# Optimization experiments

Measured on AMD Instinct MI355X. Metric: run time of the kernel, lower is better.

Reference implementation:

```python
import jax, jax.numpy as jnp
import numpy as np

NUM_HEADS = 16
HEAD_DIM = 64  # hidden_size 1024 / 16 heads


def setup_inputs() -> dict:
    key = jax.random.key(0)
    ks = jax.random.split(key, 7)
    B, S, D = 32, 577, 1024
    s = 0.02
    return {
        "hidden_states": jax.random.normal(ks[0], (B, S, D), dtype=jnp.float32),
        "Wq": jax.random.normal(ks[1], (D, D), dtype=jnp.float32) * s,
        "bq": jax.random.normal(ks[2], (D,), dtype=jnp.float32) * s,
        "Wk": jax.random.normal(ks[3], (D, D), dtype=jnp.float32) * s,
        "bk": jax.random.normal(ks[4], (D,), dtype=jnp.float32) * s,
        "Wv": jax.random.normal(ks[5], (D, D), dtype=jnp.float32) * s,
        "bv": jax.random.normal(ks[6], (D,), dtype=jnp.float32) * s,
    }


def _split_heads(x):
    # [B, S, D] -> [B, H, S, d]
    B, S, D = x.shape
    return x.reshape(B, S, NUM_HEADS, HEAD_DIM).transpose(0, 2, 1, 3)


def reference(hidden_states, Wq, bq, Wk, bk, Wv, bv):
    # torch Linear: y = x @ W^T + b
    q = _split_heads(hidden_states @ Wq.T + bq)  # [B,H,S,d]
    k = _split_heads(hidden_states @ Wk.T + bk)
    v = _split_heads(hidden_states @ Wv.T + bv)

    scale = 1.0 / np.sqrt(HEAD_DIM).astype(np.float32)
    scores = jnp.einsum("bhqd,bhkd->bhqk", q, k) * scale  # [B,H,S,S]
    probs = jax.nn.softmax(scores, axis=-1)
    ctx = jnp.einsum("bhqk,bhkd->bhqd", probs, v)  # [B,H,S,d]
    B, H, S, d = ctx.shape
    ctx = ctx.transpose(0, 2, 1, 3).reshape(B, S, H * d)  # [B,S,D]
    return ctx
```

## Files before the change

kernel.cpp:

```cpp
#include <hip/hip_runtime.h>
#include <stdint.h>

#define NB 32
#define SEQ 577
#define SPAD 640
#define NH 16
#define HD 64
#define DM 1024
#define MTOT (NB * SEQ)
#define KT_N 16

typedef __bf16 bf16x8 __attribute__((ext_vector_type(8)));
typedef float f32x4 __attribute__((ext_vector_type(4)));
typedef unsigned short u16x8 __attribute__((ext_vector_type(8)));
typedef unsigned short u16x4 __attribute__((ext_vector_type(4)));

__device__ __forceinline__ unsigned short f2bf(float f) {
  unsigned int u = __builtin_bit_cast(unsigned int, f);
  return (unsigned short)((u + 0x7FFFu + ((u >> 16) & 1u)) >> 16);
}

__device__ __forceinline__ f32x4 mfma16(bf16x8 a, bf16x8 b, f32x4 c) {
  return __builtin_amdgcn_mfma_f32_16x16x32_bf16(a, b, c, 0, 0, 0);
}

__device__ __forceinline__ void gload16(const unsigned short* g, unsigned short* l) {
  __builtin_amdgcn_global_load_lds(
      (const __attribute__((address_space(1))) unsigned int*)g,
      (__attribute__((address_space(3))) unsigned int*)l, 16, 0, 0);
}

#define BC8(p) __builtin_bit_cast(bf16x8, *(const u16x8*)(p))

#if __has_builtin(__builtin_amdgcn_exp2f)
#define EXP2(x) __builtin_amdgcn_exp2f(x)
#else
#define EXP2(x) exp2f(x)
#endif

__global__ void cvt_kernel(const float* __restrict__ x,
                           const float* __restrict__ wq,
                           const float* __restrict__ wk,
                           const float* __restrict__ wv,
                           unsigned short* __restrict__ xb,
                           unsigned short* __restrict__ wb) {
  const long long NX = (long long)MTOT * DM;
  long long i = ((long long)blockIdx.x * blockDim.x + threadIdx.x) * 4;
  const float* src;
  unsigned short* dst;
  if (i < NX) {
    src = x + i;
    dst = xb + i;
  } else {
    long long j = i - NX;
    int wsel = (int)(j >> 20);
    long long off = j & 0xFFFFF;
    src = (wsel == 0 ? wq : wsel == 1 ? wk : wv) + off;
    dst = wb + j;
  }
  f32x4 v = *(const f32x4*)src;
  u16x4 o;
  o.x = f2bf(v.x); o.y = f2bf(v.y); o.z = f2bf(v.z); o.w = f2bf(v.w);
  *(u16x4*)dst = o;
}

template <int MODE>
__device__ __forceinline__ void kloop256(
    unsigned short* LDS, const unsigned short* const* gA,
    const unsigned short* const* gB, f32x4 (&acc)[8][4],
    int rA0, int rB0, int ch0, int ch1) {
#define MM(ACC, AF, BF)                                   \
  do {                                                    \
    if constexpr (MODE == 0)                              \
      ACC = mfma16(AF, BF, ACC);                          \
    else                                                  \
      ACC = mfma16(BF, AF, ACC);                          \
  } while (0)
  const int t = threadIdx.x;
  for (int kt = 0; kt < KT_N; ++kt) {
    unsigned short* ab = LDS + (kt & 1) * 32768;
    unsigned short* bb = ab + 16384;
    const bool st = (kt + 2) < KT_N;
    const int ko2 = (kt + 2) * 64;
    bf16x8 af[4][2], bf0[2][2], bf1[2][2];

#pragma unroll
    for (int mi = 0; mi < 4; mi++) {
      const unsigned short* rp = ab + (rA0 + mi * 16) * 64;
      af[mi][0] = BC8(rp + ch0);
      af[mi][1] = BC8(rp + ch1);
    }
#pragma unroll
    for (int ni = 0; ni < 2; ni++) {
      const unsigned short* rp = bb + (rB0 + ni * 16) * 64;
      bf0[ni][0] = BC8(rp + ch0);
      bf0[ni][1] = BC8(rp + ch1);
    }
    __builtin_amdgcn_s_setprio(1);
#pragma unroll
    for (int mi = 0; mi < 4; mi++)
#pragma unroll
      for (int ni = 0; ni < 2; ni++) {
        MM(acc[mi][ni], af[mi][0], bf0[ni][0]);
        MM(acc[mi][ni], af[mi][1], bf0[ni][1]);
      }
    __builtin_amdgcn_s_setprio(0);
    asm volatile("s_waitcnt lgkmcnt(0)" ::: "memory");
    __builtin_amdgcn_s_barrier();
    __builtin_amdgcn_sched_barrier(0);

    if (st) {
      gload16(gA[0] + ko2, ab + 0 * 4096 + t * 8);
      gload16(gA[2] + ko2, ab + 2 * 4096 + t * 8);
    }
#pragma unroll
    for (int ni = 0; ni < 2; ni++) {
      const unsigned short* rp = bb + (rB0 + (2 + ni) * 16) * 64;
      bf1[ni][0] = BC8(rp + ch0);
      bf1[ni][1] = BC8(rp + ch1);
    }
    __builtin_amdgcn_s_setprio(1);
#pragma unroll
    for (int mi = 0; mi < 4; mi++)
#pragma unroll
      for (int ni = 0; ni < 2; ni++) {
        MM(acc[mi][2 + ni], af[mi][0], bf1[ni][0]);
        MM(acc[mi][2 + ni], af[mi][1], bf1[ni][1]);
      }
    __builtin_amdgcn_s_setprio(0);
    asm volatile("s_waitcnt lgkmcnt(0)" ::: "memory");
    __builtin_amdgcn_s_barrier();
    __builtin_amdgcn_sched_barrier(0);

    if (st) {
#pragma unroll
      for (int q = 0; q < 4; q++) gload16(gB[q] + ko2, bb + q * 4096 + t * 8);
    }
#pragma unroll
    for (int mi = 0; mi < 4; mi++) {
      const unsigned short* rp = ab + (rA0 + 64 + mi * 16) * 64;
      af[mi][0] = BC8(rp + ch0);
      af[mi][1] = BC8(rp + ch1);
    }
    __builtin_amdgcn_s_setprio(1);
#pragma unroll
    for (int mi = 0; mi < 4; mi++)
#pragma unroll
      for (int ni = 0; ni < 2; ni++) {
        MM(acc[4 + mi][2 + ni], af[mi][0], bf1[ni][0]);
        MM(acc[4 + mi][2 + ni], af[mi][1], bf1[ni][1]);
      }
    __builtin_amdgcn_s_setprio(0);
    asm volatile("s_waitcnt lgkmcnt(0)" ::: "memory");
    __builtin_amdgcn_s_barrier();
    __builtin_amdgcn_sched_barrier(0);

    if (st) {
      gload16(gA[1] + ko2, ab + 1 * 4096 + t * 8);
      gload16(gA[3] + ko2, ab + 3 * 4096 + t * 8);
    }
    __builtin_amdgcn_s_setprio(1);
#pragma unroll
    for (int mi = 0; mi < 4; mi++)
#pragma unroll
      for (int ni = 0; ni < 2; ni++) {
        MM(acc[4 + mi][ni], af[mi][0], bf0[ni][0]);
        MM(acc[4 + mi][ni], af[mi][1], bf0[ni][1]);
      }
    __builtin_amdgcn_s_setprio(0);
    if (kt == KT_N - 2)
      asm volatile("s_waitcnt vmcnt(0)" ::: "memory");
    else
      asm volatile("s_waitcnt vmcnt(8)" ::: "memory");
    __builtin_amdgcn_s_barrier();
    __builtin_amdgcn_sched_barrier(0);
  }
#undef MM
}

__global__ __launch_bounds__(512, 2) void gemm256u(
    const unsigned short* __restrict__ xb, const unsigned short* __restrict__ wb,
    const float* __restrict__ bq, const float* __restrict__ bk,
    const float* __restrict__ bv,
    unsigned short* __restrict__ qo, unsigned short* __restrict__ ko,
    unsigned short* __restrict__ vo) {
  __shared__ __align__(16) unsigned short LDS[65536];
  const int id = blockIdx.x;
  int m_tile, col, z;
  bool modeV;
  if (id < 584) {
    modeV = false;
    const int xcd = id & 7, j = id >> 3;
    const int p = xcd * 73 + j;
    m_tile = p >> 3;
    col = p & 7;
    z = col >> 2;
  } else {
    modeV = true;
    const int q = id - 584;
    const int xcd = q & 7, j = q >> 3;
    const int p = (xcd < 4) ? xcd * 37 + j : 148 + (xcd - 4) * 36 + j;
    m_tile = p >> 2;
    col = p & 3;
    z = 2;
  }
  const int n0 = (modeV ? col : (col & 3)) * 256;
  const int m0 = m_tile * 256;

  const int t = threadIdx.x;
  const int lane = t & 63;
  const int w = t >> 6;
  const int g = lane >> 4, c = lane & 15;
  const int wm = w & 1, wn = w >> 1;

  const unsigned short* W = wb + (size_t)z * (DM * DM);
  const float* bias = modeV ? bv : (z ? bk : bq);
  unsigned short* outp = modeV ? vo : (z ? ko : qo);

  const int srow = t >> 3;
  const int schunk = (t & 7) ^ (srow & 7);
  const unsigned short* gA[4];
#pragma unroll
  for (int q = 0; q < 4; q++) {
    int rg = m0 + q * 64 + srow;
    if (rg > MTOT - 1) rg = MTOT - 1;
    gA[q] = xb + (size_t)rg * DM + schunk * 8;
  }
  const unsigned short* gB[4];
#pragma unroll
  for (int q = 0; q < 4; q++)
    gB[q] = W + (size_t)(n0 + q * 64 + srow) * DM + schunk * 8;

  const int cx = c & 7;
  const int ch0 = (g ^ cx) * 8;
  const int ch1 = ((4 + g) ^ cx) * 8;

  f32x4 acc[8][4];
#pragma unroll
  for (int mi = 0; mi < 8; mi++)
#pragma unroll
    for (int ni = 0; ni < 4; ni++) acc[mi][ni] = (f32x4)0.0f;

#pragma unroll
  for (int q = 0; q < 4; q++) gload16(gA[q], LDS + q * 4096 + t * 8);
#pragma unroll
  for (int q = 0; q < 4; q++) gload16(gB[q], LDS + 16384 + q * 4096 + t * 8);
#pragma unroll
  for (int q = 0; q < 4; q++) gload16(gA[q] + 64, LDS + 32768 + q * 4096 + t * 8);
#pragma unroll
  for (int q = 0; q < 4; q++)
    gload16(gB[q] + 64, LDS + 32768 + 16384 + q * 4096 + t * 8);
  asm volatile("s_waitcnt vmcnt(8)" ::: "memory");
  __builtin_amdgcn_s_barrier();
  __builtin_amdgcn_sched_barrier(0);

  const int rA0 = wm * 128 + c;
  const int rB0 = wn * 64 + c;

  if (!modeV)
    kloop256<0>(LDS, gA, gB, acc, rA0, rB0, ch0, ch1);
  else
    kloop256<1>(LDS, gA, gB, acc, rA0, rB0, ch0, ch1);

  if (!modeV) {
    float bias4[4];
#pragma unroll
    for (int ni = 0; ni < 4; ni++) bias4[ni] = bias[n0 + wn * 64 + ni * 16 + c];
#pragma unroll
    for (int mi = 0; mi < 8; mi++) {
      int mb = m0 + wm * 128 + mi * 16 + g * 4;
#pragma unroll
      for (int r = 0; r < 4; r++) {
        int m = mb + r;
        if (m >= MTOT) continue;
        int bi = m / SEQ;
        int s = m - bi * SEQ;
#pragma unroll
        for (int ni = 0; ni < 4; ni++) {
          int n = n0 + wn * 64 + ni * 16 + c;
          int hh = n >> 6, dd = n & 63;
          outp[(((size_t)bi * NH + hh) * SPAD + s) * HD + dd] =
              f2bf(acc[mi][ni][r] + bias4[ni]);
        }
      }
    }
  } else {
#pragma unroll
    for (int ni = 0; ni < 4; ni++) {
#pragma unroll
      for (int r = 0; r < 4; r++) {
        int n = n0 + wn * 64 + ni * 16 + g * 4 + r;
        int hh = n >> 6, dd = n & 63;
        float bn = bias[n];
#pragma unroll
        for (int mi = 0; mi < 8; mi++) {
          int m = m0 + wm * 128 + mi * 16 + c;
          if (m >= MTOT) continue;
          int bi = m / SEQ;
          int s = m - bi * SEQ;
          outp[(((size_t)bi * NH + hh) * HD + dd) * SPAD + s] =
              f2bf(acc[mi][ni][r] + bn);
        }
      }
    }
  }
}

__global__ __launch_bounds__(256, 4) void attn_kernel(
    const unsigned short* __restrict__ Qb, const unsigned short* __restrict__ Kb,
    const unsigned short* __restrict__ Vt, float* __restrict__ out) {
  __shared__ __align__(16) unsigned short Ks[64 * 64];
  __shared__ __align__(16) unsigned short Vs[80 * 64];
  __shared__ __align__(16) unsigned short Pl[4][16 * 72];
  const int t = threadIdx.x, lane = t & 63, w = t >> 6;
  const int g = lane >> 4, c = lane & 15;

  const int id = blockIdx.x;
  const int xcd = id & 7;
  const int slot = id >> 3;
  const int qt = slot % 10;
  const int pairIdx = slot / 10;
  const int pair = xcd * 64 + pairIdx;
  const int b = pair >> 4;
  const int h = pair & 15;

  const int q0 = qt * 64 + w * 16;
  const size_t bh = (size_t)b * NH + h;
  const unsigned short* Qp = Qb + bh * SPAD * HD;
  const unsigned short* Kp = Kb + bh * SPAD * HD;
  const unsigned short* Vp = Vt + bh * HD * SPAD;

  {
    int rr = t >> 4, col = (t & 15) * 4;
    unsigned short val = (rr == 0) ? (unsigned short)0x3F80 : (unsigned short)0;
    u16x4 v4 = {val, val, val, val};
    *(u16x4*)(Vs + (64 + rr) * 64 + col) = v4;
  }

  bf16x8 qf0 = __builtin_bit_cast(
      bf16x8, *(const u16x8*)(Qp + (size_t)(q0 + c) * HD + g * 8));
  bf16x8 qf1 = __builtin_bit_cast(
      bf16x8, *(const u16x8*)(Qp + (size_t)(q0 + c) * HD + 32 + g * 8));

  const int C0 = t, C1 = t + 256;
  const int r0 = C0 >> 3, cg0 = (C0 & 7) ^ (r0 & 7);
  const int r1 = C1 >> 3, cg1 = (C1 & 7) ^ (r1 & 7);
  const unsigned short* gK0 = Kp + (size_t)(r0 * 8 + cg0) * 8;
  const unsigned short* gK1 = Kp + (size_t)(r1 * 8 + cg1) * 8;
  const unsigned short* gV0 = Vp + (size_t)r0 * SPAD + cg0 * 8;
  const unsigned short* gV1 = Vp + (size_t)r1 * SPAD + cg1 * 8;
  unsigned short* lK0 = Ks + C0 * 8;
  unsigned short* lK1 = Ks + C1 * 8;
  unsigned short* lV0 = Vs + C0 * 8;
  unsigned short* lV1 = Vs + C1 * 8;

  f32x4 oacc[5];
#pragma unroll
  for (int nt = 0; nt < 5; nt++) oacc[nt] = (f32x4)0.0f;
  unsigned short* pl = &Pl[w][0];
  const float SC = 0.125f * 1.44269504f;

  for (int kt = 0; kt < 10; kt++) {
    const int kv0 = kt * 64;
    __syncthreads();
    gload16(gK0 + kv0 * 64, lK0);
    gload16(gK1 + kv0 * 64, lK1);
    gload16(gV0 + kv0, lV0);
    gload16(gV1 + kv0, lV1);
    __syncthreads();

    f32x4 sc[4];
#pragma unroll
    for (int nt = 0; nt < 4; nt++) {
      const int row = nt * 16 + c;
      const unsigned short* kb = Ks + row * 64;
      bf16x8 k0 = __builtin_bit_cast(
          bf16x8, *(const u16x8*)(kb + ((g ^ (row & 7)) * 8)));
      bf16x8 k1 = __builtin_bit_cast(
          bf16x8, *(const u16x8*)(kb + (((4 + g) ^ (row & 7)) * 8)));
      sc[nt] = mfma16(qf0, k0, (f32x4)0.0f);
      sc[nt] = mfma16(qf1, k1, sc[nt]);
    }

    if (kt == 9) {
#pragma unroll
      for (int nt = 0; nt < 4; nt++) {
        const bool valid = (kv0 + nt * 16 + c) < SEQ;
#pragma unroll
        for (int r = 0; r < 4; r++)
          sc[nt][r] = valid ? EXP2(sc[nt][r] * SC) : 0.0f;
      }
    } else {
#pragma unroll
      for (int nt = 0; nt < 4; nt++)
#pragma unroll
        for (int r = 0; r < 4; r++) sc[nt][r] = EXP2(sc[nt][r] * SC);
    }

#pragma unroll
    for (int nt = 0; nt < 4; nt++)
#pragma unroll
      for (int r = 0; r < 4; r++)
        pl[(g * 4 + r) * 72 + nt * 16 + c] = f2bf(sc[nt][r]);
    bf16x8 pa0 = __builtin_bit_cast(bf16x8, *(const u16x8*)(pl + c * 72 + g * 8));
    bf16x8 pa1 =
        __builtin_bit_cast(bf16x8, *(const u16x8*)(pl + c * 72 + 32 + g * 8));

#pragma unroll
    for (int nt = 0; nt < 5; nt++) {
      const int row = nt * 16 + c;
      const unsigned short* vb = Vs + row * 64;
      bf16x8 v0 = __builtin_bit_cast(
          bf16x8, *(const u16x8*)(vb + ((g ^ (row & 7)) * 8)));
      bf16x8 v1 = __builtin_bit_cast(
          bf16x8, *(const u16x8*)(vb + (((4 + g) ^ (row & 7)) * 8)));
      oacc[nt] = mfma16(pa0, v0, oacc[nt]);
      oacc[nt] = mfma16(pa1, v1, oacc[nt]);
    }
  }

#pragma unroll
  for (int r = 0; r < 4; r++) {
    int s = q0 + g * 4 + r;
    if (s >= SEQ) continue;
    float l = __shfl(oacc[4][r], lane & 48, 64);
    float inv = 1.0f / l;
#pragma unroll
    for (int nt = 0; nt < 4; nt++)
      out[((size_t)b * SEQ + s) * DM + h * HD + nt * 16 + c] =
          oacc[nt][r] * inv;
  }
}

extern "C" void kernel_launch(void* const* d_in, const int* in_sizes, int n_in,
                              void* d_out, int out_size, void* d_ws,
                              size_t ws_size, hipStream_t stream) {
  const float* x = (const float*)d_in[0];
  const float* Wq = (const float*)d_in[1];
  const float* bq = (const float*)d_in[2];
  const float* Wk = (const float*)d_in[3];
  const float* bk = (const float*)d_in[4];
  const float* Wv = (const float*)d_in[5];
  const float* bv = (const float*)d_in[6];
  float* out = (float*)d_out;

  const size_t nXB = (size_t)MTOT * DM;
  const size_t nWB = (size_t)3 * DM * DM;
  const size_t nQK = (size_t)NB * NH * SPAD * HD;
  const size_t needed = (nXB + nWB + 3 * nQK) * 2;
  if (ws_size < needed) return;

  unsigned short* xb = (unsigned short*)d_ws;
  unsigned short* wb = xb + nXB;
  unsigned short* Qb = wb + nWB;
  unsigned short* Kb = Qb + nQK;
  unsigned short* Vt = Kb + nQK;

  cvt_kernel<<<21536, 256, 0, stream>>>(x, Wq, Wk, Wv, xb, wb);
  gemm256u<<<876, 512, 0, stream>>>(xb, wb, bq, bk, bv, Qb, Kb, Vt);
  attn_kernel<<<5120, 256, 0, stream>>>(Qb, Kb, Vt, out);
}
```

Measured before the change: 385.7 us.

## Double-buffer K/V tiles in attention kernel to overlap loads with MFMA

The attention kernel keeps two LDS buffers each for K and V. It prefetches the next 64-key tile while the current tile is used for QK^T, exp and PV, so the two barriers per iteration become one barrier at the end. The ones-row block used to accumulate the softmax denominator moves to its own LDS array, since it no longer sits at the end of Vs. LDS use per block grows, so the launch bounds target drops from 4 to 3 blocks per CU. That trades occupancy for hiding global-load latency.

```diff
diff --git a/kernel.cpp b/kernel.cpp
--- a/kernel.cpp
+++ b/kernel.cpp
@@ -306,11 +306,12 @@
   }
 }
 
-__global__ __launch_bounds__(256, 4) void attn_kernel(
+__global__ __launch_bounds__(256, 3) void attn_kernel(
     const unsigned short* __restrict__ Qb, const unsigned short* __restrict__ Kb,
     const unsigned short* __restrict__ Vt, float* __restrict__ out) {
-  __shared__ __align__(16) unsigned short Ks[64 * 64];
-  __shared__ __align__(16) unsigned short Vs[80 * 64];
+  __shared__ __align__(16) unsigned short Ks[2][64 * 64];
+  __shared__ __align__(16) unsigned short Vs[2][64 * 64];
+  __shared__ __align__(16) unsigned short Vones[16 * 64];
   __shared__ __align__(16) unsigned short Pl[4][16 * 72];
   const int t = threadIdx.x, lane = t & 63, w = t >> 6;
   const int g = lane >> 4, c = lane & 15;
@@ -334,7 +335,7 @@
     int rr = t >> 4, col = (t & 15) * 4;
     unsigned short val = (rr == 0) ? (unsigned short)0x3F80 : (unsigned short)0;
     u16x4 v4 = {val, val, val, val};
-    *(u16x4*)(Vs + (64 + rr) * 64 + col) = v4;
+    *(u16x4*)(Vones + rr * 64 + col) = v4;
   }
 
   bf16x8 qf0 = __builtin_bit_cast(
@@ -349,10 +350,6 @@
   const unsigned short* gK1 = Kp + (size_t)(r1 * 8 + cg1) * 8;
   const unsigned short* gV0 = Vp + (size_t)r0 * SPAD + cg0 * 8;
   const unsigned short* gV1 = Vp + (size_t)r1 * SPAD + cg1 * 8;
-  unsigned short* lK0 = Ks + C0 * 8;
-  unsigned short* lK1 = Ks + C1 * 8;
-  unsigned short* lV0 = Vs + C0 * 8;
-  unsigned short* lV1 = Vs + C1 * 8;
 
   f32x4 oacc[5];
 #pragma unroll
@@ -360,20 +357,27 @@
   unsigned short* pl = &Pl[w][0];
   const float SC = 0.125f * 1.44269504f;
 
+  gload16(gK0, Ks[0] + C0 * 8);
+  gload16(gK1, Ks[0] + C1 * 8);
+  gload16(gV0, Vs[0] + C0 * 8);
+  gload16(gV1, Vs[0] + C1 * 8);
+  __syncthreads();
+
   for (int kt = 0; kt < 10; kt++) {
-    const int kv0 = kt * 64;
-    __syncthreads();
-    gload16(gK0 + kv0 * 64, lK0);
-    gload16(gK1 + kv0 * 64, lK1);
-    gload16(gV0 + kv0, lV0);
-    gload16(gV1 + kv0, lV1);
-    __syncthreads();
+    const int cur = kt & 1, nxt = cur ^ 1;
+    if (kt < 9) {
+      const int kv1 = (kt + 1) * 64;
+      gload16(gK0 + kv1 * 64, Ks[nxt] + C0 * 8);
+      gload16(gK1 + kv1 * 64, Ks[nxt] + C1 * 8);
+      gload16(gV0 + kv1, Vs[nxt] + C0 * 8);
+      gload16(gV1 + kv1, Vs[nxt] + C1 * 8);
+    }
 
     f32x4 sc[4];
 #pragma unroll
     for (int nt = 0; nt < 4; nt++) {
       const int row = nt * 16 + c;
-      const unsigned short* kb = Ks + row * 64;
+      const unsigned short* kb = Ks[cur] + row * 64;
       bf16x8 k0 = __builtin_bit_cast(
           bf16x8, *(const u16x8*)(kb + ((g ^ (row & 7)) * 8)));
       bf16x8 k1 = __builtin_bit_cast(
@@ -383,6 +387,7 @@
     }
 
     if (kt == 9) {
+      const int kv0 = kt * 64;
 #pragma unroll
       for (int nt = 0; nt < 4; nt++) {
         const bool valid = (kv0 + nt * 16 + c) < SEQ;
@@ -409,7 +414,8 @@
 #pragma unroll
     for (int nt = 0; nt < 5; nt++) {
       const int row = nt * 16 + c;
-      const unsigned short* vb = Vs + row * 64;
+      const unsigned short* vb =
+          (nt == 4) ? (Vones + c * 64) : (Vs[cur] + row * 64);
       bf16x8 v0 = __builtin_bit_cast(
           bf16x8, *(const u16x8*)(vb + ((g ^ (row & 7)) * 8)));
       bf16x8 v1 = __builtin_bit_cast(
@@ -417,6 +423,8 @@
       oacc[nt] = mfma16(pa0, v0, oacc[nt]);
       oacc[nt] = mfma16(pa1, v1, oacc[nt]);
     }
+
+    __syncthreads();
   }
 
 #pragma unroll
```

Result: slower. 404.1 us (+4.8%).
